# Kernel optimization log

Measured on AMD Instinct MI355X. Metric: run time of the kernel, lower is better.

## Reference

```python
import jax, jax.numpy as jnp
import numpy as np

B, S, C = 8, 1024, 1280   # B = 2*N (uncond|cond halves), S = 32*32 latent tokens
H, D = 20, 64             # heads, head_dim; H*D == C


def setup_inputs() -> dict:
    key = jax.random.key(0)
    ks = jax.random.split(key, 5)
    std = 1.0 / np.sqrt(C)
    return {
        "hidden_states": jax.random.normal(ks[0], (B, S, C), jnp.float32),
        "Wq": jax.random.normal(ks[1], (C, C), jnp.float32) * std,
        "Wk": jax.random.normal(ks[2], (C, C), jnp.float32) * std,
        "Wv": jax.random.normal(ks[3], (C, C), jnp.float32) * std,
        "Wo": jax.random.normal(ks[4], (C, C), jnp.float32) * std,
        "bo": jnp.zeros((C,), jnp.float32),
    }


def _inject(x, n):
    # replicate reference rows 0 (uncond) and n (cond) across each half
    unc = jnp.broadcast_to(x[0:1], (n,) + x.shape[1:])
    con = jnp.broadcast_to(x[n:n + 1], (n,) + x.shape[1:])
    return jnp.concatenate([unc, con], axis=0)


def reference(hidden_states, Wq, Wk, Wv, Wo, bo):
    b, s, c = hidden_states.shape
    n = b // 2
    q = hidden_states @ Wq
    k = hidden_states @ Wk
    v = hidden_states @ Wv
    # PnP injection (self-attention, share_enabled, n > 1, all injections on)
    q = _inject(q, n)
    k = _inject(k, n)
    v = _inject(v, n)
    # head split: [b, s, c] -> [b, h, s, d]
    q = q.reshape(b, s, H, D).transpose(0, 2, 1, 3)
    k = k.reshape(b, s, H, D).transpose(0, 2, 1, 3)
    v = v.reshape(b, s, H, D).transpose(0, 2, 1, 3)
    scale = 1.0 / np.sqrt(D)
    scores = jnp.einsum("bhqd,bhkd->bhqk", q, k) * scale
    probs = jax.nn.softmax(scores, axis=-1)
    out = jnp.einsum("bhqk,bhkd->bhqd", probs, v)
    out = out.transpose(0, 2, 1, 3).reshape(b, s, c)
    return out @ Wo + bo
```

## Files before the change

### kernel.cpp

```cpp
#include <hip/hip_runtime.h>

#define S_LEN 1024
#define C_DIM 1280
#define NH 20
#define HD 64

typedef __attribute__((ext_vector_type(8))) short short8;
typedef __attribute__((ext_vector_type(4))) short short4v;
typedef __attribute__((ext_vector_type(4))) float float4v;

__device__ __forceinline__ float bf2f(unsigned short u) {
    union { unsigned u; float f; } v; v.u = ((unsigned)u) << 16; return v.f;
}
__device__ __forceinline__ unsigned short f2bf(float f) {
    union { float f; unsigned u; } v; v.f = f;
    unsigned u = v.u;
    return (unsigned short)((u + 0x7FFFu + ((u >> 16) & 1u)) >> 16);
}

__device__ __forceinline__ void load_lds16(const unsigned short* g, unsigned short* l) {
    __builtin_amdgcn_global_load_lds(
        (const __attribute__((address_space(1))) unsigned int*)g,
        (__attribute__((address_space(3))) unsigned int*)l, 16, 0, 0);
}

__global__ __launch_bounds__(256) void detect_kernel(
    const unsigned int* __restrict__ w, int* __restrict__ flag)
{
    __shared__ int cnt;
    if (threadIdx.x == 0) cnt = 0;
    __syncthreads();
    int local = 0;
    for (int i = threadIdx.x; i < 1024; i += 256) {
        unsigned e = (w[i] >> 7) & 0xFFu;
        if (e >= 100u && e <= 140u) local++;
    }
    atomicAdd(&cnt, local);
    __syncthreads();
    if (threadIdx.x == 0) *flag = (cnt < 512) ? 1 : 0;
}

__global__ __launch_bounds__(256) void convx_kernel(
    const void* __restrict__ hs, const int* __restrict__ flag,
    unsigned short* __restrict__ X)
{
    const size_t SC = (size_t)S_LEN * C_DIM;
    int g = blockIdx.y;
    size_t off = ((size_t)blockIdx.x * 256 + threadIdx.x) * 8;
    size_t src = (size_t)g * 4 * SC + off;
    short8 o;
    if (*flag) {
        const float* p = (const float*)hs + src;
        for (int j = 0; j < 8; j++) o[j] = (short)f2bf(p[j]);
    } else {
        o = *(const short8*)((const unsigned short*)hs + src);
    }
    *(short8*)(X + g * SC + off) = o;
}

__global__ __launch_bounds__(256) void convw_kernel(
    const void* __restrict__ Wq, const void* __restrict__ Wk,
    const void* __restrict__ Wv, const void* __restrict__ Wo,
    const int* __restrict__ flag, unsigned short* __restrict__ WT)
{
    __shared__ unsigned short tile[64 * 68];
    const void* W = (blockIdx.z == 0) ? Wq : (blockIdx.z == 1) ? Wk
                    : (blockIdx.z == 2) ? Wv : Wo;
    unsigned short* T = WT + (size_t)blockIdx.z * C_DIM * C_DIM;
    int fp32 = *flag;
    int c0 = blockIdx.x * 64, r0 = blockIdx.y * 64;
    int t = threadIdx.x;
    int r = t >> 3, cg = t & 7;
    for (int rep = 0; rep < 2; rep++) {
        int rr = r0 + r + rep * 32;
        if (fp32) {
            const float* p = (const float*)W + (size_t)rr * C_DIM + c0 + cg * 8;
            for (int j = 0; j < 8; j++)
                tile[(r + rep * 32) * 68 + cg * 8 + j] = f2bf(p[j]);
        } else {
            short8 v = *(const short8*)((const unsigned short*)W + (size_t)rr * C_DIM + c0 + cg * 8);
            for (int j = 0; j < 8; j++)
                tile[(r + rep * 32) * 68 + cg * 8 + j] = (unsigned short)v[j];
        }
    }
    __syncthreads();
    int c = t >> 3, rg = t & 7;
    for (int rep = 0; rep < 2; rep++) {
        short8 o;
        for (int j = 0; j < 8; j++)
            o[j] = (short)tile[(rg * 8 + j) * 68 + c + rep * 32];
        *(short8*)(T + (size_t)(c0 + c + rep * 32) * C_DIM + r0 + rg * 8) = o;
    }
}

__global__ __launch_bounds__(256) void gemm_qkv_kernel(
    const unsigned short* __restrict__ X,
    const unsigned short* __restrict__ WT,
    unsigned short* __restrict__ Qo, unsigned short* __restrict__ Ko,
    unsigned short* __restrict__ Vt)
{
    __shared__ __align__(16) unsigned short Al[2][128 * 64];
    __shared__ __align__(16) unsigned short Bl[2][128 * 64];
    int z = blockIdx.z;
    const unsigned short* Wt = WT + (size_t)z * C_DIM * C_DIM;
    int c0 = blockIdx.x * 128, r0 = blockIdx.y * 128;
    int t = threadIdx.x, wave = t >> 6, lane = t & 63;
    int wr = wave >> 1, wc = wave & 1, quad = lane >> 4, mn = lane & 15;
    int srow = wave * 8 + (lane >> 3), slot = lane & 7;
    const unsigned short* xb = X + (size_t)r0 * C_DIM;
    const unsigned short* wb = Wt + (size_t)c0 * C_DIM;

    auto stage = [&](int ki, int buf) {
        int k0 = ki * 64;
        for (int p = 0; p < 4; p++) {
            int row = p * 32 + srow; int ck = slot ^ (row & 7);
            load_lds16(xb + (size_t)row * C_DIM + k0 + ck * 8, &Al[buf][row * 64 + slot * 8]);
        }
        for (int p = 0; p < 4; p++) {
            int row = p * 32 + srow; int ck = slot ^ (row & 7);
            load_lds16(wb + (size_t)row * C_DIM + k0 + ck * 8, &Bl[buf][row * 64 + slot * 8]);
        }
    };

    stage(0, 0);
    asm volatile("s_waitcnt vmcnt(0)" ::: "memory");
    __builtin_amdgcn_s_barrier();

    float4v acc[4][4] = {};
    for (int kt = 0; kt < 20; kt++) {
        int cur = kt & 1, nxt = cur ^ 1;
        if (kt < 19) stage(kt + 1, nxt);
        for (int kc = 0; kc < 2; kc++) {
            short8 a[4], b[4];
            for (int mt = 0; mt < 4; mt++) {
                int row = wr * 64 + mt * 16 + mn;
                a[mt] = *(const short8*)(&Al[cur][row * 64 + (((kc * 4 + quad) ^ (row & 7)) * 8)]);
            }
            for (int nt = 0; nt < 4; nt++) {
                int row = wc * 64 + nt * 16 + mn;
                b[nt] = *(const short8*)(&Bl[cur][row * 64 + (((kc * 4 + quad) ^ (row & 7)) * 8)]);
            }
            for (int mt = 0; mt < 4; mt++)
                for (int nt = 0; nt < 4; nt++)
                    acc[mt][nt] = __builtin_amdgcn_mfma_f32_16x16x32_bf16(a[mt], b[nt], acc[mt][nt], 0, 0, 0);
        }
        asm volatile("s_waitcnt vmcnt(0)" ::: "memory");
        __builtin_amdgcn_s_barrier();
    }

    if (z == 2) {
        int g = r0 >> 10;
        for (int mt = 0; mt < 4; mt++) {
            int row = r0 + wr * 64 + mt * 16 + quad * 4;
            int s = row & 1023;
            for (int nt = 0; nt < 4; nt++) {
                int col = c0 + wc * 64 + nt * 16 + mn;
                short4v p;
                for (int i = 0; i < 4; i++) p[i] = (short)f2bf(acc[mt][nt][i]);
                *(short4v*)(Vt + ((size_t)g * C_DIM + col) * S_LEN + s) = p;
            }
        }
    } else {
        unsigned short* Out = (z == 0) ? Qo : Ko;
        for (int mt = 0; mt < 4; mt++) {
            int row = r0 + wr * 64 + mt * 16 + quad * 4;
            for (int nt = 0; nt < 4; nt++) {
                int col = c0 + wc * 64 + nt * 16 + mn;
                for (int i = 0; i < 4; i++)
                    Out[(size_t)(row + i) * C_DIM + col] = f2bf(acc[mt][nt][i]);
            }
        }
    }
}

__global__ __launch_bounds__(256) void attn_kernel(
    const unsigned short* __restrict__ Q, const unsigned short* __restrict__ K,
    const unsigned short* __restrict__ VT, unsigned short* __restrict__ O)
{
    __shared__ __align__(16) unsigned short Kl[2][64 * 64];
    __shared__ __align__(16) unsigned short Vl[2][64 * 64];
    __shared__ unsigned short Pl[4 * 16 * 72];
    int qt = blockIdx.x, h = blockIdx.y, g = blockIdx.z;
    int t = threadIdx.x, wave = t >> 6, lane = t & 63;
    int quad = lane >> 4, n = lane & 15;
    const size_t SC = (size_t)S_LEN * C_DIM;
    const unsigned short* Qb = Q + (size_t)g * SC;
    const unsigned short* Kb = K + (size_t)g * SC + h * HD;
    const unsigned short* Vb = VT + (size_t)g * SC + (size_t)(h * HD) * S_LEN;
    unsigned short* Pw = &Pl[wave * 16 * 72];

    int srow = wave * 8 + (lane >> 3);
    int slot = lane & 7;

    short8 qa[2];
    int qrow = qt * 64 + wave * 16 + n;
    for (int kc = 0; kc < 2; kc++) {
        short8 v = *(const short8*)(Qb + (size_t)qrow * C_DIM + h * HD + kc * 32 + quad * 8);
        short8 w;
        for (int j = 0; j < 8; j++)
            w[j] = (short)f2bf(bf2f((unsigned short)v[j]) * 0.125f);
        qa[kc] = w;
    }

    for (int p = 0; p < 2; p++) {
        int row = p * 32 + srow;
        int ck = slot ^ (row & 7);
        load_lds16(Kb + (size_t)row * C_DIM + ck * 8, &Kl[0][row * 64 + slot * 8]);
        load_lds16(Vb + (size_t)row * S_LEN + ck * 8, &Vl[0][row * 64 + slot * 8]);
    }
    asm volatile("s_waitcnt vmcnt(0)" ::: "memory");
    __builtin_amdgcn_s_barrier();

    float4v oacc[4] = {};
    float lsum[4] = { 0.f, 0.f, 0.f, 0.f };

    for (int kt = 0; kt < 16; kt++) {
        int cur = kt & 1, nxt = cur ^ 1;
        if (kt < 15) {
            for (int p = 0; p < 2; p++) {
                int row = p * 32 + srow;
                int ck = slot ^ (row & 7);
                load_lds16(Kb + (size_t)((kt + 1) * 64 + row) * C_DIM + ck * 8,
                           &Kl[nxt][row * 64 + slot * 8]);
                load_lds16(Vb + (size_t)row * S_LEN + (kt + 1) * 64 + ck * 8,
                           &Vl[nxt][row * 64 + slot * 8]);
            }
        }
        const unsigned short* Kt = Kl[cur];
        const unsigned short* Vt = Vl[cur];

        float4v sacc[4] = {};
        for (int kc = 0; kc < 2; kc++)
            for (int nt = 0; nt < 4; nt++) {
                int row = nt * 16 + n;
                short8 kb = *(const short8*)(Kt + row * 64 + (((kc * 4 + quad) ^ (row & 7)) * 8));
                sacc[nt] = __builtin_amdgcn_mfma_f32_16x16x32_bf16(qa[kc], kb, sacc[nt], 0, 0, 0);
            }

        for (int nt = 0; nt < 4; nt++)
            for (int i = 0; i < 4; i++) {
                float p = __expf(sacc[nt][i]);
                lsum[i] += p;
                Pw[(quad * 4 + i) * 72 + nt * 16 + n] = f2bf(p);
            }
        asm volatile("s_waitcnt lgkmcnt(0)" ::: "memory");
        short8 pa0 = *(const short8*)(&Pw[n * 72 + quad * 8]);
        short8 pa1 = *(const short8*)(&Pw[n * 72 + 32 + quad * 8]);
        for (int kc = 0; kc < 2; kc++) {
            short8 pa = kc ? pa1 : pa0;
            for (int nt = 0; nt < 4; nt++) {
                int row = nt * 16 + n;
                short8 vb = *(const short8*)(Vt + row * 64 + (((kc * 4 + quad) ^ (row & 7)) * 8));
                oacc[nt] = __builtin_amdgcn_mfma_f32_16x16x32_bf16(pa, vb, oacc[nt], 0, 0, 0);
            }
        }
        asm volatile("s_waitcnt vmcnt(0)" ::: "memory");
        __builtin_amdgcn_s_barrier();
    }

    for (int i = 0; i < 4; i++)
        for (int d = 1; d < 16; d <<= 1)
            lsum[i] += __shfl_xor(lsum[i], d, 64);
    float inv[4];
    for (int i = 0; i < 4; i++) inv[i] = 1.0f / lsum[i];

    int row0 = qt * 64 + wave * 16 + quad * 4;
    for (int nt = 0; nt < 4; nt++)
        for (int i = 0; i < 4; i++)
            O[(size_t)g * SC + (size_t)(row0 + i) * C_DIM + h * HD + nt * 16 + n] =
                f2bf(oacc[nt][i] * inv[i]);
}

__global__ __launch_bounds__(256) void gemm_out_kernel(
    const unsigned short* __restrict__ X,
    const unsigned short* __restrict__ WoT,
    const void* __restrict__ bo,
    const int* __restrict__ flag,
    void* __restrict__ out)
{
    __shared__ __align__(16) unsigned short Al[2][64 * 64];
    __shared__ __align__(16) unsigned short Bl[2][64 * 64];
    int c0 = blockIdx.x * 64, r0 = blockIdx.y * 64;
    int t = threadIdx.x, wave = t >> 6, lane = t & 63;
    int wr = wave >> 1, wc = wave & 1, quad = lane >> 4, mn = lane & 15;
    int srow = wave * 8 + (lane >> 3), slot = lane & 7;
    const unsigned short* xb = X + (size_t)r0 * C_DIM;
    const unsigned short* wb = WoT + (size_t)c0 * C_DIM;
    int fp32 = *flag;

    for (int p = 0; p < 2; p++) {
        int row = p * 32 + srow; int ck = slot ^ (row & 7);
        load_lds16(xb + (size_t)row * C_DIM + ck * 8, &Al[0][row * 64 + slot * 8]);
        load_lds16(wb + (size_t)row * C_DIM + ck * 8, &Bl[0][row * 64 + slot * 8]);
    }
    asm volatile("s_waitcnt vmcnt(0)" ::: "memory");
    __builtin_amdgcn_s_barrier();

    float4v acc[2][2] = {};
    for (int kt = 0; kt < 20; kt++) {
        int cur = kt & 1, nxt = cur ^ 1;
        if (kt < 19) {
            int k0 = (kt + 1) * 64;
            for (int p = 0; p < 2; p++) {
                int row = p * 32 + srow; int ck = slot ^ (row & 7);
                load_lds16(xb + (size_t)row * C_DIM + k0 + ck * 8, &Al[nxt][row * 64 + slot * 8]);
                load_lds16(wb + (size_t)row * C_DIM + k0 + ck * 8, &Bl[nxt][row * 64 + slot * 8]);
            }
        }
        for (int kc = 0; kc < 2; kc++) {
            short8 a[2], b[2];
            for (int mt = 0; mt < 2; mt++) {
                int row = wr * 32 + mt * 16 + mn;
                a[mt] = *(const short8*)(&Al[cur][row * 64 + (((kc * 4 + quad) ^ (row & 7)) * 8)]);
            }
            for (int nt = 0; nt < 2; nt++) {
                int row = wc * 32 + nt * 16 + mn;
                b[nt] = *(const short8*)(&Bl[cur][row * 64 + (((kc * 4 + quad) ^ (row & 7)) * 8)]);
            }
            for (int mt = 0; mt < 2; mt++)
                for (int nt = 0; nt < 2; nt++)
                    acc[mt][nt] = __builtin_amdgcn_mfma_f32_16x16x32_bf16(a[mt], b[nt], acc[mt][nt], 0, 0, 0);
        }
        asm volatile("s_waitcnt vmcnt(0)" ::: "memory");
        __builtin_amdgcn_s_barrier();
    }

    for (int mt = 0; mt < 2; mt++) {
        int row = r0 + wr * 32 + mt * 16 + quad * 4;
        int g = row >> 10;
        for (int nt = 0; nt < 2; nt++) {
            int col = c0 + wc * 32 + nt * 16 + mn;
            float bb = fp32 ? ((const float*)bo)[col] : bf2f(((const unsigned short*)bo)[col]);
            for (int i = 0; i < 4; i++) {
                float v = acc[mt][nt][i] + bb;
                int s = (row + i) & 1023;
                if (fp32) {
                    float* o = (float*)out;
                    for (int rep = 0; rep < 4; rep++)
                        o[((size_t)(g * 4 + rep) * S_LEN + s) * C_DIM + col] = v;
                } else {
                    unsigned short* o = (unsigned short*)out;
                    unsigned short bv = f2bf(v);
                    for (int rep = 0; rep < 4; rep++)
                        o[((size_t)(g * 4 + rep) * S_LEN + s) * C_DIM + col] = bv;
                }
            }
        }
    }
}

extern "C" void kernel_launch(void* const* d_in, const int* in_sizes, int n_in,
                              void* d_out, int out_size, void* d_ws, size_t ws_size,
                              hipStream_t stream)
{
    const void* hs = d_in[0];
    const void* Wq = d_in[1];
    const void* Wk = d_in[2];
    const void* Wv = d_in[3];
    const void* Wo = d_in[4];
    const void* bo = d_in[5];

    const size_t CC  = (size_t)C_DIM * C_DIM;
    const size_t SC2 = (size_t)2 * S_LEN * C_DIM;

    int* flag = (int*)d_ws;
    unsigned short* base = (unsigned short*)((char*)d_ws + 256);
    unsigned short* WT = base;
    unsigned short* X  = WT + 4 * CC;
    unsigned short* Q  = X + SC2;
    unsigned short* K  = Q + SC2;
    unsigned short* VT = K + SC2;

    hipLaunchKernelGGL(detect_kernel, dim3(1), dim3(256), 0, stream,
                       (const unsigned int*)Wq, flag);
    hipLaunchKernelGGL(convx_kernel, dim3(640, 2), dim3(256), 0, stream,
                       hs, flag, X);
    hipLaunchKernelGGL(convw_kernel, dim3(20, 20, 4), dim3(256), 0, stream,
                       Wq, Wk, Wv, Wo, flag, WT);
    hipLaunchKernelGGL(gemm_qkv_kernel, dim3(10, 16, 3), dim3(256), 0, stream,
                       X, WT, Q, K, VT);
    hipLaunchKernelGGL(attn_kernel, dim3(16, NH, 2), dim3(256), 0, stream,
                       Q, K, VT, X );
    hipLaunchKernelGGL(gemm_out_kernel, dim3(20, 32), dim3(256), 0, stream,
                       X, WT + 3 * CC, bo, flag, d_out);
}
```

Before: 207.1 us.

## Remove detect kernel, remap grids for XCD locality, load QKV B-operand directly

Drops the separate dtype-detect launch and has each kernel detect fp32 inline with a wave ballot over 64 words of Wq. The QKV GEMM, attention and output GEMM grids are flattened to 1D with block index remapping, apparently so blocks sharing operands land on the same XCD (lin&7) and reuse its L2. The QKV GEMM also stops staging the weight tile in LDS and reads B fragments straight from global memory into registers. This saves one launch and half the LDS, but direct global loads of B are uncoalesced, 16-byte-per-lane reads exposed in the inner loop.

Result: slower. 215.1 us (+3.8%).

```diff
diff --git a/kernel.cpp b/kernel.cpp
--- a/kernel.cpp
+++ b/kernel.cpp
@@ -24,32 +24,24 @@
         (__attribute__((address_space(3))) unsigned int*)l, 16, 0, 0);
 }
 
-__global__ __launch_bounds__(256) void detect_kernel(
-    const unsigned int* __restrict__ w, int* __restrict__ flag)
-{
-    __shared__ int cnt;
-    if (threadIdx.x == 0) cnt = 0;
-    __syncthreads();
-    int local = 0;
-    for (int i = threadIdx.x; i < 1024; i += 256) {
-        unsigned e = (w[i] >> 7) & 0xFFu;
-        if (e >= 100u && e <= 140u) local++;
-    }
-    atomicAdd(&cnt, local);
-    __syncthreads();
-    if (threadIdx.x == 0) *flag = (cnt < 512) ? 1 : 0;
+__device__ __forceinline__ int detect_fp32(const unsigned int* wq) {
+    unsigned u = wq[threadIdx.x & 63];
+    unsigned e = (u >> 7) & 0xFFu;
+    unsigned long long m = __ballot(e >= 100u && e <= 140u);
+    return __popcll(m) < 32;
 }
 
 __global__ __launch_bounds__(256) void convx_kernel(
-    const void* __restrict__ hs, const int* __restrict__ flag,
+    const void* __restrict__ hs, const unsigned int* __restrict__ wq,
     unsigned short* __restrict__ X)
 {
+    int fp32 = detect_fp32(wq);
     const size_t SC = (size_t)S_LEN * C_DIM;
     int g = blockIdx.y;
     size_t off = ((size_t)blockIdx.x * 256 + threadIdx.x) * 8;
     size_t src = (size_t)g * 4 * SC + off;
     short8 o;
-    if (*flag) {
+    if (fp32) {
         const float* p = (const float*)hs + src;
         for (int j = 0; j < 8; j++) o[j] = (short)f2bf(p[j]);
     } else {
@@ -61,13 +53,13 @@
 __global__ __launch_bounds__(256) void convw_kernel(
     const void* __restrict__ Wq, const void* __restrict__ Wk,
     const void* __restrict__ Wv, const void* __restrict__ Wo,
-    const int* __restrict__ flag, unsigned short* __restrict__ WT)
+    unsigned short* __restrict__ WT)
 {
     __shared__ unsigned short tile[64 * 68];
+    int fp32 = detect_fp32((const unsigned int*)Wq);
     const void* W = (blockIdx.z == 0) ? Wq : (blockIdx.z == 1) ? Wk
                     : (blockIdx.z == 2) ? Wv : Wo;
     unsigned short* T = WT + (size_t)blockIdx.z * C_DIM * C_DIM;
-    int fp32 = *flag;
     int c0 = blockIdx.x * 64, r0 = blockIdx.y * 64;
     int t = threadIdx.x;
     int r = t >> 3, cg = t & 7;
@@ -100,49 +92,55 @@
     unsigned short* __restrict__ Vt)
 {
     __shared__ __align__(16) unsigned short Al[2][128 * 64];
-    __shared__ __align__(16) unsigned short Bl[2][128 * 64];
-    int z = blockIdx.z;
+    int lin = blockIdx.x;
+    int r = lin & 7, j = lin >> 3;
+    int pl = j >> 4, y = j & 15;
+    int p = pl * 8 + r;
+    if (p >= 30) {
+        int idx = (r - 6) * 12 + (j - 48);
+        p = 24 + (idx >> 2);
+        y = 12 + (idx & 3);
+    }
+    int x = p % 10, z = p / 10;
+    int c0 = x * 128, r0 = y * 128;
+
     const unsigned short* Wt = WT + (size_t)z * C_DIM * C_DIM;
-    int c0 = blockIdx.x * 128, r0 = blockIdx.y * 128;
     int t = threadIdx.x, wave = t >> 6, lane = t & 63;
     int wr = wave >> 1, wc = wave & 1, quad = lane >> 4, mn = lane & 15;
     int srow = wave * 8 + (lane >> 3), slot = lane & 7;
     const unsigned short* xb = X + (size_t)r0 * C_DIM;
-    const unsigned short* wb = Wt + (size_t)c0 * C_DIM;
-
-    auto stage = [&](int ki, int buf) {
+    const unsigned short* wb = Wt + (size_t)(c0 + wc * 64 + mn) * C_DIM + quad * 8;
+
+    auto stageA = [&](int ki, int buf) {
         int k0 = ki * 64;
-        for (int p = 0; p < 4; p++) {
-            int row = p * 32 + srow; int ck = slot ^ (row & 7);
+        for (int q = 0; q < 4; q++) {
+            int row = q * 32 + srow; int ck = slot ^ (row & 7);
             load_lds16(xb + (size_t)row * C_DIM + k0 + ck * 8, &Al[buf][row * 64 + slot * 8]);
         }
-        for (int p = 0; p < 4; p++) {
-            int row = p * 32 + srow; int ck = slot ^ (row & 7);
-            load_lds16(wb + (size_t)row * C_DIM + k0 + ck * 8, &Bl[buf][row * 64 + slot * 8]);
-        }
     };
 
-    stage(0, 0);
+    stageA(0, 0);
     asm volatile("s_waitcnt vmcnt(0)" ::: "memory");
     __builtin_amdgcn_s_barrier();
 
     float4v acc[4][4] = {};
     for (int kt = 0; kt < 20; kt++) {
         int cur = kt & 1, nxt = cur ^ 1;
-        if (kt < 19) stage(kt + 1, nxt);
+        if (kt < 19) stageA(kt + 1, nxt);
+        int k0 = kt * 64;
+        short8 b[2][4];
+        for (int kc = 0; kc < 2; kc++)
+            for (int nt = 0; nt < 4; nt++)
+                b[kc][nt] = *(const short8*)(wb + (size_t)(nt * 16) * C_DIM + k0 + kc * 32);
         for (int kc = 0; kc < 2; kc++) {
-            short8 a[4], b[4];
+            short8 a[4];
             for (int mt = 0; mt < 4; mt++) {
                 int row = wr * 64 + mt * 16 + mn;
                 a[mt] = *(const short8*)(&Al[cur][row * 64 + (((kc * 4 + quad) ^ (row & 7)) * 8)]);
             }
-            for (int nt = 0; nt < 4; nt++) {
-                int row = wc * 64 + nt * 16 + mn;
-                b[nt] = *(const short8*)(&Bl[cur][row * 64 + (((kc * 4 + quad) ^ (row & 7)) * 8)]);
-            }
             for (int mt = 0; mt < 4; mt++)
                 for (int nt = 0; nt < 4; nt++)
-                    acc[mt][nt] = __builtin_amdgcn_mfma_f32_16x16x32_bf16(a[mt], b[nt], acc[mt][nt], 0, 0, 0);
+                    acc[mt][nt] = __builtin_amdgcn_mfma_f32_16x16x32_bf16(a[mt], b[kc][nt], acc[mt][nt], 0, 0, 0);
         }
         asm volatile("s_waitcnt vmcnt(0)" ::: "memory");
         __builtin_amdgcn_s_barrier();
@@ -155,9 +153,9 @@
             int s = row & 1023;
             for (int nt = 0; nt < 4; nt++) {
                 int col = c0 + wc * 64 + nt * 16 + mn;
-                short4v p;
-                for (int i = 0; i < 4; i++) p[i] = (short)f2bf(acc[mt][nt][i]);
-                *(short4v*)(Vt + ((size_t)g * C_DIM + col) * S_LEN + s) = p;
+                short4v pk;
+                for (int i = 0; i < 4; i++) pk[i] = (short)f2bf(acc[mt][nt][i]);
+                *(short4v*)(Vt + ((size_t)g * C_DIM + col) * S_LEN + s) = pk;
             }
         }
     } else {
@@ -180,7 +178,12 @@
     __shared__ __align__(16) unsigned short Kl[2][64 * 64];
     __shared__ __align__(16) unsigned short Vl[2][64 * 64];
     __shared__ unsigned short Pl[4 * 16 * 72];
-    int qt = blockIdx.x, h = blockIdx.y, g = blockIdx.z;
+    int lin = blockIdx.x;
+    int r = lin & 7, j = lin >> 3;
+    int m = j >> 4, qt = j & 15;
+    int pair = r + 8 * m;
+    int h = pair % 20, g = pair / 20;
+
     int t = threadIdx.x, wave = t >> 6, lane = t & 63;
     int quad = lane >> 4, n = lane & 15;
     const size_t SC = (size_t)S_LEN * C_DIM;
@@ -197,13 +200,13 @@
     for (int kc = 0; kc < 2; kc++) {
         short8 v = *(const short8*)(Qb + (size_t)qrow * C_DIM + h * HD + kc * 32 + quad * 8);
         short8 w;
-        for (int j = 0; j < 8; j++)
-            w[j] = (short)f2bf(bf2f((unsigned short)v[j]) * 0.125f);
+        for (int jj = 0; jj < 8; jj++)
+            w[jj] = (short)f2bf(bf2f((unsigned short)v[jj]) * 0.125f);
         qa[kc] = w;
     }
 
-    for (int p = 0; p < 2; p++) {
-        int row = p * 32 + srow;
+    for (int q = 0; q < 2; q++) {
+        int row = q * 32 + srow;
         int ck = slot ^ (row & 7);
         load_lds16(Kb + (size_t)row * C_DIM + ck * 8, &Kl[0][row * 64 + slot * 8]);
         load_lds16(Vb + (size_t)row * S_LEN + ck * 8, &Vl[0][row * 64 + slot * 8]);
@@ -217,8 +220,8 @@
     for (int kt = 0; kt < 16; kt++) {
         int cur = kt & 1, nxt = cur ^ 1;
         if (kt < 15) {
-            for (int p = 0; p < 2; p++) {
-                int row = p * 32 + srow;
+            for (int q = 0; q < 2; q++) {
+                int row = q * 32 + srow;
                 int ck = slot ^ (row & 7);
                 load_lds16(Kb + (size_t)((kt + 1) * 64 + row) * C_DIM + ck * 8,
                            &Kl[nxt][row * 64 + slot * 8]);
@@ -239,9 +242,9 @@
 
         for (int nt = 0; nt < 4; nt++)
             for (int i = 0; i < 4; i++) {
-                float p = __expf(sacc[nt][i]);
-                lsum[i] += p;
-                Pw[(quad * 4 + i) * 72 + nt * 16 + n] = f2bf(p);
+                float pv = __expf(sacc[nt][i]);
+                lsum[i] += pv;
+                Pw[(quad * 4 + i) * 72 + nt * 16 + n] = f2bf(pv);
             }
         asm volatile("s_waitcnt lgkmcnt(0)" ::: "memory");
         short8 pa0 = *(const short8*)(&Pw[n * 72 + quad * 8]);
@@ -275,21 +278,31 @@
     const unsigned short* __restrict__ X,
     const unsigned short* __restrict__ WoT,
     const void* __restrict__ bo,
-    const int* __restrict__ flag,
+    const unsigned int* __restrict__ wq,
     void* __restrict__ out)
 {
     __shared__ __align__(16) unsigned short Al[2][64 * 64];
     __shared__ __align__(16) unsigned short Bl[2][64 * 64];
-    int c0 = blockIdx.x * 64, r0 = blockIdx.y * 64;
+    int fp32 = detect_fp32(wq);
+    int lin = blockIdx.x;
+    int x, y;
+    if (lin < 512) {
+        int r = lin & 7, j = lin >> 3;
+        x = r + 8 * (j >> 5); y = j & 31;
+    } else {
+        int idx = lin - 512;
+        x = 16 + (idx >> 5); y = idx & 31;
+    }
+    int c0 = x * 64, r0 = y * 64;
+
     int t = threadIdx.x, wave = t >> 6, lane = t & 63;
     int wr = wave >> 1, wc = wave & 1, quad = lane >> 4, mn = lane & 15;
     int srow = wave * 8 + (lane >> 3), slot = lane & 7;
     const unsigned short* xb = X + (size_t)r0 * C_DIM;
     const unsigned short* wb = WoT + (size_t)c0 * C_DIM;
-    int fp32 = *flag;
-
-    for (int p = 0; p < 2; p++) {
-        int row = p * 32 + srow; int ck = slot ^ (row & 7);
+
+    for (int q = 0; q < 2; q++) {
+        int row = q * 32 + srow; int ck = slot ^ (row & 7);
         load_lds16(xb + (size_t)row * C_DIM + ck * 8, &Al[0][row * 64 + slot * 8]);
         load_lds16(wb + (size_t)row * C_DIM + ck * 8, &Bl[0][row * 64 + slot * 8]);
     }
@@ -301,8 +314,8 @@
         int cur = kt & 1, nxt = cur ^ 1;
         if (kt < 19) {
             int k0 = (kt + 1) * 64;
-            for (int p = 0; p < 2; p++) {
-                int row = p * 32 + srow; int ck = slot ^ (row & 7);
+            for (int q = 0; q < 2; q++) {
+                int row = q * 32 + srow; int ck = slot ^ (row & 7);
                 load_lds16(xb + (size_t)row * C_DIM + k0 + ck * 8, &Al[nxt][row * 64 + slot * 8]);
                 load_lds16(wb + (size_t)row * C_DIM + k0 + ck * 8, &Bl[nxt][row * 64 + slot * 8]);
             }
@@ -363,24 +376,21 @@
     const size_t CC  = (size_t)C_DIM * C_DIM;
     const size_t SC2 = (size_t)2 * S_LEN * C_DIM;
 
-    int* flag = (int*)d_ws;
-    unsigned short* base = (unsigned short*)((char*)d_ws + 256);
+    unsigned short* base = (unsigned short*)d_ws;
     unsigned short* WT = base;
     unsigned short* X  = WT + 4 * CC;
     unsigned short* Q  = X + SC2;
     unsigned short* K  = Q + SC2;
     unsigned short* VT = K + SC2;
 
-    hipLaunchKernelGGL(detect_kernel, dim3(1), dim3(256), 0, stream,
-                       (const unsigned int*)Wq, flag);
     hipLaunchKernelGGL(convx_kernel, dim3(640, 2), dim3(256), 0, stream,
-                       hs, flag, X);
+                       hs, (const unsigned int*)Wq, X);
     hipLaunchKernelGGL(convw_kernel, dim3(20, 20, 4), dim3(256), 0, stream,
-                       Wq, Wk, Wv, Wo, flag, WT);
-    hipLaunchKernelGGL(gemm_qkv_kernel, dim3(10, 16, 3), dim3(256), 0, stream,
+                       Wq, Wk, Wv, Wo, WT);
+    hipLaunchKernelGGL(gemm_qkv_kernel, dim3(480), dim3(256), 0, stream,
                        X, WT, Q, K, VT);
-    hipLaunchKernelGGL(attn_kernel, dim3(16, NH, 2), dim3(256), 0, stream,
+    hipLaunchKernelGGL(attn_kernel, dim3(640), dim3(256), 0, stream,
                        Q, K, VT, X );
-    hipLaunchKernelGGL(gemm_out_kernel, dim3(20, 32), dim3(256), 0, stream,
-                       X, WT + 3 * CC, bo, flag, d_out);
-}
+    hipLaunchKernelGGL(gemm_out_kernel, dim3(640), dim3(256), 0, stream,
+                       X, WT + 3 * CC, bo, (const unsigned int*)Wq, d_out);
+}
```
